# Optimization experiments

Hardware: AMD Instinct MI355X
Metric: run time of the kernel (lower is better)

The kernel has to match this reference:

```python
import jax, jax.numpy as jnp
import numpy as np

B, C, H, W = 4, 64, 64, 64
RC, RS = 8, 4  # channel reduction, spatial reduction
CR = C // RC
KS = 2 * RS - 1  # 7


def _conv(x, w, b, stride, pad):
    y = jax.lax.conv_general_dilated(
        x, w, (stride, stride), [(pad, pad), (pad, pad)],
        dimension_numbers=('NCHW', 'OIHW', 'NCHW'))
    return y + b[None, :, None, None]


def setup_inputs() -> dict:
    key = jax.random.key(0)
    ks = jax.random.split(key, 13)

    def w_init(k, shape):
        fan_in = shape[1] * shape[2] * shape[3]
        return jax.random.normal(k, shape, jnp.float32) / jnp.sqrt(fan_in)

    x = jax.random.normal(ks[0], (B, C, H, W), jnp.float32)
    return {
        'x': x,
        'w1': w_init(ks[1], (CR, C, 1, 1)), 'b1': jnp.zeros((CR,), jnp.float32),
        'w2': w_init(ks[2], (CR, C, 1, 1)), 'b2': jnp.zeros((CR,), jnp.float32),
        'w3': w_init(ks[3], (C, C, 1, 1)),  'b3': jnp.zeros((C,), jnp.float32),
        'w4': w_init(ks[4], (C, C, KS, KS)), 'b4': jnp.zeros((C,), jnp.float32),
        'w5': w_init(ks[5], (C, C, KS, KS)), 'b5': jnp.zeros((C,), jnp.float32),
        'w6': w_init(ks[6], (C, C, 1, 1)),  'b6': jnp.zeros((C,), jnp.float32),
    }


def reference(x, w1, b1, w2, b2, w3, b3, w4, b4, w5, b5, w6, b6):
    gamma = 1.0
    x_ori = x
    b, c, h, w = x.shape
    n = h * w

    # ---- Block 1: spatial self-attention (SAGAN-style), N x N scores ----
    f = _conv(x, w1, b1, 1, 0).reshape(b, CR, n)   # [B, C/8, N]
    g = _conv(x, w2, b2, 1, 0).reshape(b, CR, n)   # [B, C/8, N]
    hh = _conv(x, w3, b3, 1, 0).reshape(b, c, n)   # [B, C, N]
    s = jnp.einsum('bci,bcj->bij', f, g)           # [B, N, N] = f^T g
    beta = jax.nn.softmax(s, axis=1)               # softmax over dim 1 (as in torch)
    o = jnp.einsum('bcn,bnm->bcm', hh, beta)       # [B, C, N]
    x2 = o.reshape(b, c, h, w)

    # ---- Block 2: channel attention over strided-conv features, C x C scores ----
    hp, wp = h // RS, w // RS
    npix = hp * wp
    f2 = _conv(x2, w4, b4, RS, RS - 1).reshape(b, c, npix)  # [B, C, N']
    g2 = _conv(x2, w5, b5, RS, RS - 1).reshape(b, c, npix)  # [B, C, N']
    h2 = _conv(x2, w6, b6, 1, 0).reshape(b, c, n)           # [B, C, N]
    s2 = jnp.einsum('bcn,bdn->bcd', f2, g2)                 # [B, C, C] = f g^T
    beta2 = jax.nn.softmax(s2, axis=1)
    # o[b,d,n] = sum_c h2[b,c,n] * beta2[b,c,d]
    o2 = jnp.einsum('bcn,bcd->bdn', h2, beta2).reshape(b, c, h, w)

    return gamma * o2 + x_ori
```

## Files before the change

### kernel.cpp

```cpp
#include <hip/hip_runtime.h>
#include <math.h>

#define BB 4
#define CC 64
#define CRR 8
#define NN 4096

typedef __attribute__((ext_vector_type(8))) short bf16x8;
typedef __attribute__((ext_vector_type(4))) float f32x4;

__device__ inline float bf2f(ushort u) {
    union { uint i; float f; } v; v.i = (uint)u << 16; return v.f;
}
__device__ inline ushort f2bf(float f) {
    uint u = __builtin_bit_cast(uint, f);
    u = (u + 0x7FFFu + ((u >> 16) & 1u)) >> 16;
    return (ushort)u;
}
__device__ inline uint bfpack2(float a, float b) {
    uint ua = __builtin_bit_cast(uint, a);
    uint ub = __builtin_bit_cast(uint, b);
    ua = (ua + 0x7FFFu + ((ua >> 16) & 1u)) >> 16;
    ub = (ub + 0x7FFFu + ((ub >> 16) & 1u)) & 0xFFFF0000u;
    return ua | ub;
}
__device__ inline uint pkrtz(float a, float b) {
    return __builtin_amdgcn_perm(__builtin_bit_cast(uint, b),
                                 __builtin_bit_cast(uint, a), 0x07060302u);
}
__device__ inline float fexp2(float x) {
#if __has_builtin(__builtin_amdgcn_exp2f)
    return __builtin_amdgcn_exp2f(x);
#else
    float r; asm("v_exp_f32 %0, %1" : "=v"(r) : "v"(x)); return r;
#endif
}

#define X2P_B 313600

__global__ __launch_bounds__(256) void produce_fgh(
    const float* __restrict__ x,
    const float* __restrict__ w1, const float* __restrict__ b1,
    const float* __restrict__ w2, const float* __restrict__ b2,
    const float* __restrict__ w3, const float* __restrict__ b3,
    ushort* __restrict__ fT, ushort* __restrict__ gT, ushort* __restrict__ hhb)
{
    const float LOG2E = 1.4426950408889634f;
    int t = threadIdx.x;
    int b = blockIdx.x & 3;
    int n = ((blockIdx.x >> 2) << 6) + (t & 63);
    int og = __builtin_amdgcn_readfirstlane(t >> 6);

    const float* xb = x + ((size_t)b << 18) + n;
    float xv[64];
#pragma unroll
    for (int c = 0; c < 64; ++c) xv[c] = xb[(size_t)c << 12];

    if (og == 0) {
        ushort fo[8], go[8];
#pragma unroll
        for (int k = 0; k < 8; ++k) {
            float a1 = b1[k], a2 = b2[k];
#pragma unroll
            for (int c = 0; c < 64; ++c) {
                a1 = fmaf(w1[k * 64 + c], xv[c], a1);
                a2 = fmaf(w2[k * 64 + c], xv[c], a2);
            }
            fo[k] = f2bf(a1 * LOG2E); go[k] = f2bf(a2);
        }
        uint4 fq = make_uint4((uint)fo[0] | ((uint)fo[1] << 16),
                              (uint)fo[2] | ((uint)fo[3] << 16),
                              (uint)fo[4] | ((uint)fo[5] << 16),
                              (uint)fo[6] | ((uint)fo[7] << 16));
        uint4 gq = make_uint4((uint)go[0] | ((uint)go[1] << 16),
                              (uint)go[2] | ((uint)go[3] << 16),
                              (uint)go[4] | ((uint)go[5] << 16),
                              (uint)go[6] | ((uint)go[7] << 16));
        *(uint4*)&fT[((size_t)b << 15) + (size_t)n * 8] = fq;
        *(uint4*)&gT[((size_t)b << 15) + (size_t)n * 8] = gq;
#pragma unroll
        for (int k = 0; k < 4; ++k) {
            float a = b3[k];
#pragma unroll
            for (int c = 0; c < 64; ++c) a = fmaf(w3[k * 64 + c], xv[c], a);
            hhb[((size_t)b << 18) + ((size_t)k << 12) + n] = f2bf(a);
        }
    } else {
        int c0 = og * 20 - 16;
#pragma unroll
        for (int k = 0; k < 20; ++k) {
            float a = b3[c0 + k];
#pragma unroll
            for (int c = 0; c < 64; ++c) a = fmaf(w3[(c0 + k) * 64 + c], xv[c], a);
            hhb[((size_t)b << 18) + ((size_t)(c0 + k) << 12) + n] = f2bf(a);
        }
    }
}

__global__ __launch_bounds__(256) void wtz_kernel(
    const float* __restrict__ w4, const float* __restrict__ w5,
    const float* __restrict__ w6,
    ushort* __restrict__ Wt, ushort* __restrict__ w6b, ushort* __restrict__ x2p)
{
    int bid = blockIdx.x;
    int t = threadIdx.x;
    if (bid < 128) {
        int conv = bid >> 6, co = bid & 63;
        const float* W = conv ? w5 : w4;
        for (int i = t; i < 3136; i += 256) {
            int ci = i / 49, kk = i - ci * 49;
            Wt[(((size_t)(conv * 64 + co)) * 49 + kk) * 64 + ci] = f2bf(W[co * 3136 + i]);
        }
    } else if (bid == 128) {
#pragma unroll
        for (int k = 0; k < 16; ++k) {
            int i = k * 256 + t;
            w6b[i] = f2bf(w6[i]);
        }
    } else {
        int gid = (bid - 129) * 256 + t;
        if (gid >= 4 * 804) return;
        int b = gid / 804;
        int i = gid - b * 804;
        int py, px;
        if (i < 210) { py = i / 70; px = i - py * 70; }
        else if (i < 420) { int j = i - 210; int r = j / 70; py = 67 + r; px = j - r * 70; }
        else { int j = i - 420; int r = j / 6; py = 3 + r; int c = j - r * 6; px = c < 3 ? c : 64 + c; }
        ushort* p = x2p + (size_t)b * X2P_B + (size_t)(py * 70 + px) * 64;
        uint4 z = make_uint4(0, 0, 0, 0);
#pragma unroll
        for (int k = 0; k < 8; ++k) *(uint4*)(p + k * 8) = z;
    }
}

__global__ __launch_bounds__(1024) void attn_kernel(
    const ushort* __restrict__ fT, const ushort* __restrict__ gT,
    const ushort* __restrict__ hhb, const ushort* __restrict__ w6b,
    const float* __restrict__ b6,
    ushort* __restrict__ x2p, ushort* __restrict__ h2b)
{
    __shared__ __align__(16) char smem[79872];
    ushort* hhT = (ushort*)smem;
    ushort* PstB = (ushort*)(smem + 32768);
    float* Acc = (float*)smem;
    float* Lq  = (float*)(smem + 69632);
    ushort* x2s = (ushort*)(smem + 70656);

    int t = threadIdx.x;
    int q = t >> 8, tq = t & 255;
    int l = t & 63;
    int wq = tq >> 6;
    int w16 = t >> 6;
    int ml = l & 15, g = l >> 4;
    int b = blockIdx.x & 3;
    int mt = blockIdx.x >> 2;
    int m0 = mt << 6;
    int col = m0 + wq * 16 + ml;

    const ushort* fTb = fT + ((size_t)b << 15) + (size_t)q * 8192;
    const ushort* gTb = gT + ((size_t)b << 15);
    const ushort* hhB = hhb + ((size_t)b << 18) + (q << 10);

    const bf16x8 z8 = {0, 0, 0, 0, 0, 0, 0, 0};
    const f32x4 z4 = {0.f, 0.f, 0.f, 0.f};

    bf16x8 gfrag = *(const bf16x8*)(gTb + (size_t)col * 8);
    if (g != 0) gfrag = z8;

    int sc = tq >> 2, sp = tq & 3;
    const ushort* hrowBase = hhB + (size_t)sc * 4096 + sp * 16;
    int hdst = q * 4096 + sp * 1024 + sc * 8;

    uint4 h0 = *(const uint4*)(hrowBase);
    uint4 h1 = *(const uint4*)(hrowBase + 8);
    *(uint4*)&hhT[hdst] = h0;
    *(uint4*)&hhT[hdst + 512] = h1;
    bf16x8 afc[4];
#pragma unroll
    for (int s = 0; s < 4; ++s)
        afc[s] = *(const bf16x8*)(fTb + (size_t)(16 * s + ml) * 8);

    f32x4 acc[4] = {z4, z4, z4, z4};
    float rsum = 0.f;
    int swz = (ml & 7) << 4;
    char* pbase = (char*)PstB + w16 * 2048;
    __syncthreads();

    for (int nt = 0; nt < 16; ++nt) {
        bf16x8 afn[4];
        if (nt < 15) {
            int n0 = (nt + 1) << 6;
            h0 = *(const uint4*)(hrowBase + n0);
            h1 = *(const uint4*)(hrowBase + n0 + 8);
#pragma unroll
            for (int s = 0; s < 4; ++s)
                afn[s] = *(const bf16x8*)(fTb + (size_t)(n0 + 16 * s + ml) * 8);
        }

        f32x4 Sv[4];
#pragma unroll
        for (int s = 0; s < 4; ++s)
            Sv[s] = __builtin_amdgcn_mfma_f32_16x16x32_bf16(afc[s], gfrag, z4, 0, 0, 0);

        uint plo[4], phi[4];
#pragma unroll
        for (int s = 0; s < 4; ++s) {
            float p0 = fexp2(Sv[s][0]);
            float p1 = fexp2(Sv[s][1]);
            float p2 = fexp2(Sv[s][2]);
            float p3 = fexp2(Sv[s][3]);
            rsum += (p0 + p1) + (p2 + p3);
            plo[s] = pkrtz(p0, p1);
            phi[s] = pkrtz(p2, p3);
        }

#pragma unroll
        for (int s = 0; s < 4; ++s) {
            uint off = (uint)((ml * 128 + 32 * s + 8 * g) ^ swz);
            *(uint2*)(pbase + off) = make_uint2(plo[s], phi[s]);
        }

#pragma unroll
        for (int kk = 0; kk < 2; ++kk) {
            uint off = (uint)((ml * 128 + 64 * kk + 16 * g) ^ swz);
            bf16x8 pf = *(const bf16x8*)(pbase + off);
#pragma unroll
            for (int ct = 0; ct < 4; ++ct) {
                bf16x8 hf = *(const bf16x8*)&hhT[q * 4096 + (kk * 4 + g) * 512 + (16 * ct + ml) * 8];
                acc[ct] = __builtin_amdgcn_mfma_f32_16x16x32_bf16(hf, pf, acc[ct], 0, 0, 0);
            }
        }

        __syncthreads();
        if (nt < 15) {
            *(uint4*)&hhT[hdst] = h0;
            *(uint4*)&hhT[hdst + 512] = h1;
#pragma unroll
            for (int s = 0; s < 4; ++s) afc[s] = afn[s];
            __syncthreads();
        }
    }

    rsum += __shfl_xor(rsum, 16);
    rsum += __shfl_xor(rsum, 32);

    {
        float* arow = Acc + q * 4352 + (wq * 16 + ml) * 68;
#pragma unroll
        for (int ct = 0; ct < 4; ++ct)
            *(f32x4*)(arow + 16 * ct + 4 * g) = acc[ct];
        if (g == 0) Lq[q * 64 + wq * 16 + ml] = rsum;
    }
    __syncthreads();

    {
        int m = t >> 4, c0 = (t & 15) << 2;
        float Ltot = Lq[m] + Lq[64 + m] + Lq[128 + m] + Lq[192 + m];
        float rL = 1.f / Ltot;
        f32x4 v0 = *(const f32x4*)(Acc + 0 * 4352 + m * 68 + c0);
        f32x4 v1 = *(const f32x4*)(Acc + 1 * 4352 + m * 68 + c0);
        f32x4 v2 = *(const f32x4*)(Acc + 2 * 4352 + m * 68 + c0);
        f32x4 v3 = *(const f32x4*)(Acc + 3 * 4352 + m * 68 + c0);
        f32x4 v;
#pragma unroll
        for (int r = 0; r < 4; ++r)
            v[r] = ((v0[r] + v1[r]) + (v2[r] + v3[r])) * rL;
        uint2 pk = make_uint2(bfpack2(v[0], v[1]), bfpack2(v[2], v[3]));
        int px = m + 3, py = mt + 3;
        *(uint2*)(x2p + (size_t)b * X2P_B + (size_t)(py * 70 + px) * 64 + c0) = pk;
        *(uint2*)(x2s + m * 72 + c0) = pk;
    }
    __syncthreads();

    {
        int dt = w16 & 3, mq = w16 >> 2;
        f32x4 hacc = z4;
#pragma unroll
        for (int kk = 0; kk < 2; ++kk) {
            bf16x8 xf = *(const bf16x8*)(x2s + (mq * 16 + ml) * 72 + 32 * kk + 8 * g);
            bf16x8 wf = *(const bf16x8*)(w6b + (size_t)(16 * dt + ml) * 64 + 32 * kk + 8 * g);
            hacc = __builtin_amdgcn_mfma_f32_16x16x32_bf16(wf, xf, hacc, 0, 0, 0);
        }
        ushort* h2row = h2b + ((size_t)b << 18) + (m0 + mq * 16 + ml);
#pragma unroll
        for (int r = 0; r < 4; ++r) {
            int d = 16 * dt + 4 * g + r;
            h2row[(size_t)d << 12] = f2bf(hacc[r] + b6[d]);
        }
    }
}

__global__ __launch_bounds__(448) void conv7_kernel(
    const ushort* __restrict__ x2p, const ushort* __restrict__ Wt,
    const float* __restrict__ b4, const float* __restrict__ b5,
    float* __restrict__ f2, float* __restrict__ g2)
{
    __shared__ float red[7][512];
    int t = threadIdx.x;
    int l = t & 63, ky = t >> 6;
    int ml = l & 15, g = l >> 4;
    int bid = blockIdx.x;
    int bc = bid & 7;
    int sub = bid >> 3;
    int ct = sub & 3, oh = sub >> 2;
    int conv = bc & 1, b = bc >> 1;

    int co0 = ct * 16;
    const ushort* wb = Wt + (size_t)conv * 200704
                     + (size_t)(co0 + ml) * 3136 + (size_t)(ky * 7) * 64 + g * 8;
    const ushort* xbase = x2p + (size_t)b * X2P_B + g * 8;

    int pixoff[2];
#pragma unroll
    for (int s = 0; s < 2; ++s) {
        int opix = oh * 32 + s * 16 + ml;
        int oy = opix >> 4, ox = opix & 15;
        pixoff[s] = ((oy * 4 + ky) * 70 + ox * 4) * 64;
    }

    const f32x4 z4 = {0.f, 0.f, 0.f, 0.f};
    f32x4 acc[2] = {z4, z4};

#pragma unroll
    for (int kx = 0; kx < 7; ++kx) {
#pragma unroll
        for (int ci0 = 0; ci0 < 64; ci0 += 32) {
            bf16x8 av = *(const bf16x8*)(wb + kx * 64 + ci0);
#pragma unroll
            for (int s = 0; s < 2; ++s) {
                bf16x8 bv = *(const bf16x8*)(xbase + pixoff[s] + kx * 64 + ci0);
                acc[s] = __builtin_amdgcn_mfma_f32_16x16x32_bf16(av, bv, acc[s], 0, 0, 0);
            }
        }
    }

#pragma unroll
    for (int s = 0; s < 2; ++s)
#pragma unroll
        for (int r = 0; r < 4; ++r)
            red[ky][(4 * g + r) * 32 + s * 16 + ml] = acc[s][r];
    __syncthreads();

    const float* bias = conv ? b5 : b4;
    float* y = conv ? g2 : f2;
    for (int idx = t; idx < 512; idx += 448) {
        float s = red[0][idx];
        s += red[1][idx]; s += red[2][idx]; s += red[3][idx];
        s += red[4][idx]; s += red[5][idx]; s += red[6][idx];
        int co = co0 + (idx >> 5);
        int opix = oh * 32 + (idx & 31);
        y[((size_t)(b * 64 + co) << 8) + opix] = s + bias[co];
    }
}

__global__ __launch_bounds__(256) void s2_softmax_kernel(
    const float* __restrict__ f2, const float* __restrict__ g2,
    float* __restrict__ beta2)
{
    __shared__ __align__(16) float g2t[256][8];
    __shared__ __align__(16) float part[16][64][4];
    __shared__ __align__(16) float s2f[64][4];
    __shared__ float mx4[4], rs4[4];
    int t = threadIdx.x;
    int b = blockIdx.x & 3;
    int d0 = (blockIdx.x >> 2) << 2;

    {
        int dd = t & 3, n0 = (t >> 2) << 2;
        const float* gp = g2 + ((size_t)(b * 64 + d0 + dd) << 8) + n0;
        float4 v = *(const float4*)gp;
        g2t[n0 + 0][dd] = v.x; g2t[n0 + 1][dd] = v.y;
        g2t[n0 + 2][dd] = v.z; g2t[n0 + 3][dd] = v.w;
    }
    __syncthreads();

    int c0 = (t & 15) << 2, nq = t >> 4;
    float acc[4][4];
#pragma unroll
    for (int i = 0; i < 4; ++i)
#pragma unroll
        for (int j = 0; j < 4; ++j) acc[i][j] = 0.f;
    const float* fb = f2 + ((size_t)(b * 64) << 8);
#pragma unroll 4
    for (int i = 0; i < 16; ++i) {
        int n = (nq << 4) + ((i + nq) & 15);
        float4 gv = *(const float4*)&g2t[n][0];
        float fv0 = fb[(c0 + 0) * 256 + n];
        float fv1 = fb[(c0 + 1) * 256 + n];
        float fv2 = fb[(c0 + 2) * 256 + n];
        float fv3 = fb[(c0 + 3) * 256 + n];
        acc[0][0] = fmaf(fv0, gv.x, acc[0][0]); acc[0][1] = fmaf(fv0, gv.y, acc[0][1]);
        acc[0][2] = fmaf(fv0, gv.z, acc[0][2]); acc[0][3] = fmaf(fv0, gv.w, acc[0][3]);
        acc[1][0] = fmaf(fv1, gv.x, acc[1][0]); acc[1][1] = fmaf(fv1, gv.y, acc[1][1]);
        acc[1][2] = fmaf(fv1, gv.z, acc[1][2]); acc[1][3] = fmaf(fv1, gv.w, acc[1][3]);
        acc[2][0] = fmaf(fv2, gv.x, acc[2][0]); acc[2][1] = fmaf(fv2, gv.y, acc[2][1]);
        acc[2][2] = fmaf(fv2, gv.z, acc[2][2]); acc[2][3] = fmaf(fv2, gv.w, acc[2][3]);
        acc[3][0] = fmaf(fv3, gv.x, acc[3][0]); acc[3][1] = fmaf(fv3, gv.y, acc[3][1]);
        acc[3][2] = fmaf(fv3, gv.z, acc[3][2]); acc[3][3] = fmaf(fv3, gv.w, acc[3][3]);
    }
#pragma unroll
    for (int i = 0; i < 4; ++i)
        *(float4*)&part[nq][c0 + i][0] =
            make_float4(acc[i][0], acc[i][1], acc[i][2], acc[i][3]);
    __syncthreads();

    if (t < 64) {
        int c = t;
        float4 s = make_float4(0.f, 0.f, 0.f, 0.f);
#pragma unroll
        for (int q2 = 0; q2 < 16; ++q2) {
            float4 v = *(const float4*)&part[q2][c][0];
            s.x += v.x; s.y += v.y; s.z += v.z; s.w += v.w;
        }
        *(float4*)&s2f[c][0] = s;
    }
    __syncthreads();
    if (t < 4) {
        float mxv = s2f[0][t];
        for (int c = 1; c < 64; ++c) mxv = fmaxf(mxv, s2f[c][t]);
        float sm = 0.f;
        for (int c = 0; c < 64; ++c) sm += __expf(s2f[c][t] - mxv);
        mx4[t] = mxv; rs4[t] = 1.f / sm;
    }
    __syncthreads();
    {
        int c = t >> 2, dd = t & 3;
        beta2[((size_t)b << 12) + c * 64 + d0 + dd] =
            __expf(s2f[c][dd] - mx4[dd]) * rs4[dd];
    }
}

__global__ __launch_bounds__(256) void o2_residual_kernel(
    const ushort* __restrict__ h2b, const float* __restrict__ beta2,
    const float* __restrict__ x, float* __restrict__ out)
{
    __shared__ __align__(16) ushort bt[64][68];
    __shared__ __align__(16) ushort btl[64][68];
    __shared__ __align__(16) ushort hn[64][68];
    int t = threadIdx.x;
    int b = blockIdx.x & 3;
    int n0 = (blockIdx.x >> 2) << 6;
    int l = t & 63, w = t >> 6;
    int ml = l & 15, g = l >> 4;

    {
        int c = t >> 2, o16 = (t & 3) << 4;
        const float* bp = beta2 + ((size_t)b << 12) + c * 64 + o16;
#pragma unroll
        for (int i = 0; i < 16; i += 4) {
            float4 v = *(const float4*)(bp + i);
            float vv[4] = {v.x, v.y, v.z, v.w};
#pragma unroll
            for (int k = 0; k < 4; ++k) {
                ushort hi = f2bf(vv[k]);
                bt[o16 + i + k][c] = hi;
                btl[o16 + i + k][c] = f2bf(vv[k] - bf2f(hi));
            }
        }
        const ushort* hp = h2b + ((size_t)(b * 64 + c) << 12) + n0 + o16;
#pragma unroll
        for (int i = 0; i < 16; i += 8) {
            uint4 hv = *(const uint4*)(hp + i);
            const ushort* hs = (const ushort*)&hv;
#pragma unroll
            for (int k = 0; k < 8; ++k) hn[o16 + i + k][c] = hs[k];
        }
    }
    __syncthreads();

    const f32x4 z4 = {0.f, 0.f, 0.f, 0.f};
    f32x4 acc[4] = {z4, z4, z4, z4};
#pragma unroll
    for (int kk = 0; kk < 2; ++kk) {
        bf16x8 ah = *(const bf16x8*)&bt[w * 16 + ml][kk * 32 + g * 8];
        bf16x8 al = *(const bf16x8*)&btl[w * 16 + ml][kk * 32 + g * 8];
#pragma unroll
        for (int nt = 0; nt < 4; ++nt) {
            bf16x8 bv = *(const bf16x8*)&hn[nt * 16 + ml][kk * 32 + g * 8];
            acc[nt] = __builtin_amdgcn_mfma_f32_16x16x32_bf16(ah, bv, acc[nt], 0, 0, 0);
            acc[nt] = __builtin_amdgcn_mfma_f32_16x16x32_bf16(al, bv, acc[nt], 0, 0, 0);
        }
    }

#pragma unroll
    for (int nt = 0; nt < 4; ++nt)
#pragma unroll
        for (int r = 0; r < 4; ++r) {
            int d = w * 16 + g * 4 + r;
            int n = n0 + nt * 16 + ml;
            size_t o = ((size_t)(b * 64 + d) << 12) + n;
            out[o] = acc[nt][r] + x[o];
        }
}

extern "C" void kernel_launch(void* const* d_in, const int* in_sizes, int n_in,
                              void* d_out, int out_size, void* d_ws, size_t ws_size,
                              hipStream_t stream)
{
    const float* x  = (const float*)d_in[0];
    const float* w1 = (const float*)d_in[1];
    const float* b1 = (const float*)d_in[2];
    const float* w2 = (const float*)d_in[3];
    const float* b2 = (const float*)d_in[4];
    const float* w3 = (const float*)d_in[5];
    const float* b3 = (const float*)d_in[6];
    const float* w4 = (const float*)d_in[7];
    const float* b4 = (const float*)d_in[8];
    const float* w5 = (const float*)d_in[9];
    const float* b5 = (const float*)d_in[10];
    const float* w6 = (const float*)d_in[11];
    const float* b6 = (const float*)d_in[12];
    float* out = (float*)d_out;

    ushort* u = (ushort*)d_ws;
    ushort* fT  = u;
    ushort* gT  = fT + 131072;
    ushort* hhb = gT + 131072;
    ushort* x2p = hhb + 1048576;
    ushort* h2b = x2p + 1254400;
    ushort* Wt  = h2b + 1048576;
    ushort* w6b = Wt + 401408;
    float* fr    = (float*)(w6b + 4096);
    float* f2    = fr;
    float* g2    = fr + 65536;
    float* beta2 = fr + 131072;

    produce_fgh<<<256, 256, 0, stream>>>(x, w1, b1, w2, b2, w3, b3, fT, gT, hhb);
    wtz_kernel<<<142, 256, 0, stream>>>(w4, w5, w6, Wt, w6b, x2p);
    attn_kernel<<<256, 1024, 0, stream>>>(fT, gT, hhb, w6b, b6, x2p, h2b);
    conv7_kernel<<<256, 448, 0, stream>>>(x2p, Wt, b4, b5, f2, g2);
    s2_softmax_kernel<<<64, 256, 0, stream>>>(f2, g2, beta2);
    o2_residual_kernel<<<256, 256, 0, stream>>>(h2b, beta2, x, out);
}
```

Baseline: 75.12 us.

## Restructure spatial attention so each wave owns a key slice with private LDS

The attention kernel moves from 1024 threads, where four groups split keys and all waves share tiles, to 512 threads with 8 waves. Each wave owns a 512-key slice and computes all 64 query columns with a 4x4 accumulator tile per channel tile. The hh tiles and probability tiles now live in wave-private LDS, so the per-iteration block barriers go away and the f and h fragments are reused across four query tiles. In exchange the kernel uses much more LDS (about 147KB, which likely allows only one block per CU) and more accumulator registers, and it needs a larger 8-way cross-wave reduction at the end.

```diff
diff --git a/kernel.cpp b/kernel.cpp
--- a/kernel.cpp
+++ b/kernel.cpp
@@ -133,159 +133,173 @@
     }
 }
 
-__global__ __launch_bounds__(1024) void attn_kernel(
+__global__ __launch_bounds__(512) void attn_kernel(
     const ushort* __restrict__ fT, const ushort* __restrict__ gT,
     const ushort* __restrict__ hhb, const ushort* __restrict__ w6b,
     const float* __restrict__ b6,
     ushort* __restrict__ x2p, ushort* __restrict__ h2b)
 {
-    __shared__ __align__(16) char smem[79872];
-    ushort* hhT = (ushort*)smem;
-    ushort* PstB = (ushort*)(smem + 32768);
+    __shared__ __align__(16) char smem[150528];
+    ushort* hhW = (ushort*)smem;
+    ushort* Pw  = (ushort*)(smem + 65536);
     float* Acc = (float*)smem;
-    float* Lq  = (float*)(smem + 69632);
-    ushort* x2s = (ushort*)(smem + 70656);
+    float* Lq  = (float*)(smem + 139264);
+    ushort* x2s = (ushort*)(smem + 141312);
 
     int t = threadIdx.x;
-    int q = t >> 8, tq = t & 255;
-    int l = t & 63;
-    int wq = tq >> 6;
-    int w16 = t >> 6;
+    int w = t >> 6, l = t & 63;
     int ml = l & 15, g = l >> 4;
     int b = blockIdx.x & 3;
-    int mt = blockIdx.x >> 2;
-    int m0 = mt << 6;
-    int col = m0 + wq * 16 + ml;
-
-    const ushort* fTb = fT + ((size_t)b << 15) + (size_t)q * 8192;
+    int mt0 = blockIdx.x >> 2;
+    int m0 = mt0 << 6;
+
+    const ushort* fTb = fT + ((size_t)b << 15) + (size_t)(w * 512) * 8;
     const ushort* gTb = gT + ((size_t)b << 15);
-    const ushort* hhB = hhb + ((size_t)b << 18) + (q << 10);
+    const ushort* hrow = hhb + ((size_t)b << 18) + (size_t)l * 4096 + w * 512;
 
     const bf16x8 z8 = {0, 0, 0, 0, 0, 0, 0, 0};
     const f32x4 z4 = {0.f, 0.f, 0.f, 0.f};
 
-    bf16x8 gfrag = *(const bf16x8*)(gTb + (size_t)col * 8);
-    if (g != 0) gfrag = z8;
-
-    int sc = tq >> 2, sp = tq & 3;
-    const ushort* hrowBase = hhB + (size_t)sc * 4096 + sp * 16;
-    int hdst = q * 4096 + sp * 1024 + sc * 8;
-
-    uint4 h0 = *(const uint4*)(hrowBase);
-    uint4 h1 = *(const uint4*)(hrowBase + 8);
-    *(uint4*)&hhT[hdst] = h0;
-    *(uint4*)&hhT[hdst + 512] = h1;
+    bf16x8 gfrag[4];
+#pragma unroll
+    for (int mt = 0; mt < 4; ++mt) {
+        gfrag[mt] = *(const bf16x8*)(gTb + (size_t)(m0 + 16 * mt + ml) * 8);
+        if (g != 0) gfrag[mt] = z8;
+    }
+
+    ushort* hhme = hhW + w * 4096;
+    char* pme = (char*)(Pw + w * 4096);
+    int swz = (ml & 7) << 4;
+
+    uint4 hreg[8];
+#pragma unroll
+    for (int i = 0; i < 8; ++i) hreg[i] = *(const uint4*)(hrow + i * 8);
     bf16x8 afc[4];
 #pragma unroll
-    for (int s = 0; s < 4; ++s)
-        afc[s] = *(const bf16x8*)(fTb + (size_t)(16 * s + ml) * 8);
-
-    f32x4 acc[4] = {z4, z4, z4, z4};
-    float rsum = 0.f;
-    int swz = (ml & 7) << 4;
-    char* pbase = (char*)PstB + w16 * 2048;
-    __syncthreads();
-
-    for (int nt = 0; nt < 16; ++nt) {
+    for (int nt = 0; nt < 4; ++nt)
+        afc[nt] = *(const bf16x8*)(fTb + (size_t)(16 * nt + ml) * 8);
+#pragma unroll
+    for (int i = 0; i < 8; ++i) *(uint4*)&hhme[i * 512 + l * 8] = hreg[i];
+
+    f32x4 acc[4][4];
+#pragma unroll
+    for (int ct = 0; ct < 4; ++ct)
+#pragma unroll
+        for (int mt = 0; mt < 4; ++mt) acc[ct][mt] = z4;
+    float rsum[4] = {0.f, 0.f, 0.f, 0.f};
+
+    for (int bk = 0; bk < 8; ++bk) {
+        uint4 hnx[8];
         bf16x8 afn[4];
-        if (nt < 15) {
-            int n0 = (nt + 1) << 6;
-            h0 = *(const uint4*)(hrowBase + n0);
-            h1 = *(const uint4*)(hrowBase + n0 + 8);
-#pragma unroll
-            for (int s = 0; s < 4; ++s)
-                afn[s] = *(const bf16x8*)(fTb + (size_t)(n0 + 16 * s + ml) * 8);
-        }
-
-        f32x4 Sv[4];
-#pragma unroll
-        for (int s = 0; s < 4; ++s)
-            Sv[s] = __builtin_amdgcn_mfma_f32_16x16x32_bf16(afc[s], gfrag, z4, 0, 0, 0);
-
-        uint plo[4], phi[4];
-#pragma unroll
-        for (int s = 0; s < 4; ++s) {
-            float p0 = fexp2(Sv[s][0]);
-            float p1 = fexp2(Sv[s][1]);
-            float p2 = fexp2(Sv[s][2]);
-            float p3 = fexp2(Sv[s][3]);
-            rsum += (p0 + p1) + (p2 + p3);
-            plo[s] = pkrtz(p0, p1);
-            phi[s] = pkrtz(p2, p3);
-        }
-
-#pragma unroll
-        for (int s = 0; s < 4; ++s) {
-            uint off = (uint)((ml * 128 + 32 * s + 8 * g) ^ swz);
-            *(uint2*)(pbase + off) = make_uint2(plo[s], phi[s]);
+        if (bk < 7) {
+            int base = (bk + 1) * 64;
+#pragma unroll
+            for (int i = 0; i < 8; ++i)
+                hnx[i] = *(const uint4*)(hrow + base + i * 8);
+#pragma unroll
+            for (int nt = 0; nt < 4; ++nt)
+                afn[nt] = *(const bf16x8*)(fTb + (size_t)(base + 16 * nt + ml) * 8);
+        }
+
+#pragma unroll
+        for (int nt = 0; nt < 4; ++nt) {
+#pragma unroll
+            for (int mt = 0; mt < 4; ++mt) {
+                f32x4 Sv = __builtin_amdgcn_mfma_f32_16x16x32_bf16(
+                    afc[nt], gfrag[mt], z4, 0, 0, 0);
+                float p0 = fexp2(Sv[0]);
+                float p1 = fexp2(Sv[1]);
+                float p2 = fexp2(Sv[2]);
+                float p3 = fexp2(Sv[3]);
+                rsum[mt] += (p0 + p1) + (p2 + p3);
+                uint off = (uint)(((16 * mt + ml) * 128 + (16 * nt + 4 * g) * 2) ^ swz);
+                *(uint2*)(pme + off) = make_uint2(pkrtz(p0, p1), pkrtz(p2, p3));
+            }
         }
 
 #pragma unroll
         for (int kk = 0; kk < 2; ++kk) {
-            uint off = (uint)((ml * 128 + 64 * kk + 16 * g) ^ swz);
-            bf16x8 pf = *(const bf16x8*)(pbase + off);
-#pragma unroll
-            for (int ct = 0; ct < 4; ++ct) {
-                bf16x8 hf = *(const bf16x8*)&hhT[q * 4096 + (kk * 4 + g) * 512 + (16 * ct + ml) * 8];
-                acc[ct] = __builtin_amdgcn_mfma_f32_16x16x32_bf16(hf, pf, acc[ct], 0, 0, 0);
-            }
-        }
-
-        __syncthreads();
-        if (nt < 15) {
-            *(uint4*)&hhT[hdst] = h0;
-            *(uint4*)&hhT[hdst + 512] = h1;
-#pragma unroll
-            for (int s = 0; s < 4; ++s) afc[s] = afn[s];
-            __syncthreads();
-        }
-    }
-
-    rsum += __shfl_xor(rsum, 16);
-    rsum += __shfl_xor(rsum, 32);
+#pragma unroll
+            for (int mt = 0; mt < 4; ++mt) {
+                uint off = (uint)(((16 * mt + ml) * 128 + (32 * kk + 8 * g) * 2) ^ swz);
+                bf16x8 pf = *(const bf16x8*)(pme + off);
+#pragma unroll
+                for (int ct = 0; ct < 4; ++ct) {
+                    bf16x8 hf = *(const bf16x8*)&hhme[(kk * 4 + g) * 512 + (16 * ct + ml) * 8];
+                    acc[ct][mt] = __builtin_amdgcn_mfma_f32_16x16x32_bf16(
+                        hf, pf, acc[ct][mt], 0, 0, 0);
+                }
+            }
+        }
+
+        if (bk < 7) {
+#pragma unroll
+            for (int i = 0; i < 8; ++i) *(uint4*)&hhme[i * 512 + l * 8] = hnx[i];
+#pragma unroll
+            for (int nt = 0; nt < 4; ++nt) afc[nt] = afn[nt];
+        }
+    }
+
+#pragma unroll
+    for (int mt = 0; mt < 4; ++mt) {
+        rsum[mt] += __shfl_xor(rsum[mt], 16);
+        rsum[mt] += __shfl_xor(rsum[mt], 32);
+    }
+
+    __syncthreads();
+
+#pragma unroll
+    for (int ct = 0; ct < 4; ++ct)
+#pragma unroll
+        for (int mt = 0; mt < 4; ++mt)
+            *(f32x4*)&Acc[(size_t)(w * 64 + 16 * mt + ml) * 68 + 16 * ct + 4 * g] = acc[ct][mt];
+    if (g == 0) {
+#pragma unroll
+        for (int mt = 0; mt < 4; ++mt) Lq[w * 64 + 16 * mt + ml] = rsum[mt];
+    }
+    __syncthreads();
 
     {
-        float* arow = Acc + q * 4352 + (wq * 16 + ml) * 68;
-#pragma unroll
-        for (int ct = 0; ct < 4; ++ct)
-            *(f32x4*)(arow + 16 * ct + 4 * g) = acc[ct];
-        if (g == 0) Lq[q * 64 + wq * 16 + ml] = rsum;
+        int m = t >> 3, c0 = (t & 7) << 3;
+        float Lt = 0.f;
+#pragma unroll
+        for (int wv = 0; wv < 8; ++wv) Lt += Lq[wv * 64 + m];
+        float rL = 1.f / Lt;
+        f32x4 sa = z4, sb = z4;
+#pragma unroll
+        for (int wv = 0; wv < 8; ++wv) {
+            const float* ap = &Acc[(size_t)(wv * 64 + m) * 68 + c0];
+            sa += *(const f32x4*)ap;
+            sb += *(const f32x4*)(ap + 4);
+        }
+        uint4 pk = make_uint4(bfpack2(sa[0] * rL, sa[1] * rL),
+                              bfpack2(sa[2] * rL, sa[3] * rL),
+                              bfpack2(sb[0] * rL, sb[1] * rL),
+                              bfpack2(sb[2] * rL, sb[3] * rL));
+        int px = m + 3, py = mt0 + 3;
+        *(uint4*)(x2p + (size_t)b * X2P_B + (size_t)(py * 70 + px) * 64 + c0) = pk;
+        *(uint4*)&x2s[m * 72 + c0] = pk;
     }
     __syncthreads();
 
     {
-        int m = t >> 4, c0 = (t & 15) << 2;
-        float Ltot = Lq[m] + Lq[64 + m] + Lq[128 + m] + Lq[192 + m];
-        float rL = 1.f / Ltot;
-        f32x4 v0 = *(const f32x4*)(Acc + 0 * 4352 + m * 68 + c0);
-        f32x4 v1 = *(const f32x4*)(Acc + 1 * 4352 + m * 68 + c0);
-        f32x4 v2 = *(const f32x4*)(Acc + 2 * 4352 + m * 68 + c0);
-        f32x4 v3 = *(const f32x4*)(Acc + 3 * 4352 + m * 68 + c0);
-        f32x4 v;
-#pragma unroll
-        for (int r = 0; r < 4; ++r)
-            v[r] = ((v0[r] + v1[r]) + (v2[r] + v3[r])) * rL;
-        uint2 pk = make_uint2(bfpack2(v[0], v[1]), bfpack2(v[2], v[3]));
-        int px = m + 3, py = mt + 3;
-        *(uint2*)(x2p + (size_t)b * X2P_B + (size_t)(py * 70 + px) * 64 + c0) = pk;
-        *(uint2*)(x2s + m * 72 + c0) = pk;
-    }
-    __syncthreads();
-
-    {
-        int dt = w16 & 3, mq = w16 >> 2;
-        f32x4 hacc = z4;
-#pragma unroll
-        for (int kk = 0; kk < 2; ++kk) {
-            bf16x8 xf = *(const bf16x8*)(x2s + (mq * 16 + ml) * 72 + 32 * kk + 8 * g);
-            bf16x8 wf = *(const bf16x8*)(w6b + (size_t)(16 * dt + ml) * 64 + 32 * kk + 8 * g);
-            hacc = __builtin_amdgcn_mfma_f32_16x16x32_bf16(wf, xf, hacc, 0, 0, 0);
-        }
-        ushort* h2row = h2b + ((size_t)b << 18) + (m0 + mq * 16 + ml);
-#pragma unroll
-        for (int r = 0; r < 4; ++r) {
-            int d = 16 * dt + 4 * g + r;
-            h2row[(size_t)d << 12] = f2bf(hacc[r] + b6[d]);
+        int dt = w >> 1;
+#pragma unroll
+        for (int mi = 0; mi < 2; ++mi) {
+            int mq = (w & 1) * 2 + mi;
+            f32x4 hacc = z4;
+#pragma unroll
+            for (int kk = 0; kk < 2; ++kk) {
+                bf16x8 xf = *(const bf16x8*)&x2s[(mq * 16 + ml) * 72 + 32 * kk + 8 * g];
+                bf16x8 wf = *(const bf16x8*)(w6b + (size_t)(16 * dt + ml) * 64 + 32 * kk + 8 * g);
+                hacc = __builtin_amdgcn_mfma_f32_16x16x32_bf16(wf, xf, hacc, 0, 0, 0);
+            }
+            ushort* h2row = h2b + ((size_t)b << 18) + (m0 + mq * 16 + ml);
+#pragma unroll
+            for (int r = 0; r < 4; ++r) {
+                int d = 16 * dt + 4 * g + r;
+                h2row[(size_t)d << 12] = f2bf(hacc[r] + b6[d]);
+            }
         }
     }
 }
@@ -527,7 +541,7 @@
 
     produce_fgh<<<256, 256, 0, stream>>>(x, w1, b1, w2, b2, w3, b3, fT, gT, hhb);
     wtz_kernel<<<142, 256, 0, stream>>>(w4, w5, w6, Wt, w6b, x2p);
-    attn_kernel<<<256, 1024, 0, stream>>>(fT, gT, hhb, w6b, b6, x2p, h2b);
+    attn_kernel<<<256, 512, 0, stream>>>(fT, gT, hhb, w6b, b6, x2p, h2b);
     conv7_kernel<<<256, 448, 0, stream>>>(x2p, Wt, b4, b5, f2, g2);
     s2_softmax_kernel<<<64, 256, 0, stream>>>(f2, g2, beta2);
     o2_residual_kernel<<<256, 256, 0, stream>>>(h2b, beta2, x, out);
```

New measurement: 78.45 us. +4.4%, slower.
